# Performance work log

Measured on AMD Instinct MI355X. Metric: run time of the kernel, lower is better.

## Reference

```python
import jax, jax.numpy as jnp
import numpy as np

B, T, V, E = 1024, 100, 9173, 100
H1, H2 = 128, 512


def _gru(x, k, rk, b):
    # Keras GRU v2 (reset_after=True). x: [B,T,D], k: [D,3H], rk: [H,3H], b: [2,3H]
    bi, br = b[0], b[1]
    xs = jnp.swapaxes(jnp.einsum('btd,dh->bth', x, k) + bi, 0, 1)  # [T,B,3H]
    H = rk.shape[0]
    h0 = jnp.zeros((x.shape[0], H), x.dtype)

    def step(h, xt):
        inner = h @ rk + br
        xz, xr, xh = jnp.split(xt, 3, -1)
        rz, rr, rh = jnp.split(inner, 3, -1)
        z = jax.nn.sigmoid(xz + rz)
        r = jax.nn.sigmoid(xr + rr)
        hh = jnp.tanh(xh + r * rh)
        h = z * h + (1.0 - z) * hh
        return h, h

    _, ys = jax.lax.scan(step, h0, xs)
    return jnp.swapaxes(ys, 0, 1)  # [B,T,H]


def _lstm(x, k, rk, b, reverse=False):
    # Keras LSTM, gate order i,f,c,o. x: [B,T,D], k: [D,4H], rk: [H,4H], b: [4H]
    if reverse:
        x = x[:, ::-1]
    xs = jnp.swapaxes(jnp.einsum('btd,dh->bth', x, k) + b, 0, 1)  # [T,B,4H]
    H = rk.shape[0]
    Bb = x.shape[0]
    carry0 = (jnp.zeros((Bb, H), x.dtype), jnp.zeros((Bb, H), x.dtype))

    def step(carry, xt):
        h, c = carry
        g = xt + h @ rk
        i, f, cc, o = jnp.split(g, 4, -1)
        c = jax.nn.sigmoid(f) * c + jax.nn.sigmoid(i) * jnp.tanh(cc)
        h = jax.nn.sigmoid(o) * jnp.tanh(c)
        return (h, c), h

    _, ys = jax.lax.scan(step, carry0, xs)
    ys = jnp.swapaxes(ys, 0, 1)
    if reverse:
        ys = ys[:, ::-1]  # Bidirectional re-reverses backward outputs
    return ys


def setup_inputs() -> dict:
    key = jax.random.key(0)
    ks = jax.random.split(key, 32)
    s = 0.05
    p = {}
    p['text'] = jax.random.randint(ks[0], (B, T), 0, V)
    p['upvote'] = jax.random.normal(ks[1], (B, 1), jnp.float32)
    p['emb'] = s * jax.random.normal(ks[2], (V, E), jnp.float32)
    # forward GRU(128)
    p['gf_k'] = s * jax.random.normal(ks[3], (E, 3 * H1), jnp.float32)
    p['gf_rk'] = s * jax.random.normal(ks[4], (H1, 3 * H1), jnp.float32)
    p['gf_b'] = s * jax.random.normal(ks[5], (2, 3 * H1), jnp.float32)
    # backward LSTM(128)
    p['lb_k'] = s * jax.random.normal(ks[6], (E, 4 * H1), jnp.float32)
    p['lb_rk'] = s * jax.random.normal(ks[7], (H1, 4 * H1), jnp.float32)
    p['lb_b'] = s * jax.random.normal(ks[8], (4 * H1,), jnp.float32)
    # GRU(512) on concat(256)
    p['g2_k'] = s * jax.random.normal(ks[9], (2 * H1, 3 * H2), jnp.float32)
    p['g2_rk'] = s * jax.random.normal(ks[10], (H2, 3 * H2), jnp.float32)
    p['g2_b'] = s * jax.random.normal(ks[11], (2, 3 * H2), jnp.float32)
    # LSTM(512)
    p['l2_k'] = s * jax.random.normal(ks[12], (H2, 4 * H2), jnp.float32)
    p['l2_rk'] = s * jax.random.normal(ks[13], (H2, 4 * H2), jnp.float32)
    p['l2_b'] = s * jax.random.normal(ks[14], (4 * H2,), jnp.float32)
    # dense heads
    p['fc1_w'] = s * jax.random.normal(ks[15], (1, 512), jnp.float32)
    p['fc1_b'] = jnp.zeros((512,), jnp.float32)
    p['d1_w'] = s * jax.random.normal(ks[16], (1024, 64), jnp.float32)
    p['d1_b'] = jnp.zeros((64,), jnp.float32)
    p['d2_w'] = s * jax.random.normal(ks[17], (64, 512), jnp.float32)
    p['d2_b'] = jnp.zeros((512,), jnp.float32)
    p['d3_w'] = s * jax.random.normal(ks[18], (512, 128), jnp.float32)
    p['d3_b'] = jnp.zeros((128,), jnp.float32)
    p['rat_w'] = s * jax.random.normal(ks[19], (128, 5), jnp.float32)
    p['rat_b'] = jnp.zeros((5,), jnp.float32)
    p['rec_w'] = s * jax.random.normal(ks[20], (128, 1), jnp.float32)
    p['rec_b'] = jnp.zeros((1,), jnp.float32)
    return p


def reference(text, upvote, emb, gf_k, gf_rk, gf_b, lb_k, lb_rk, lb_b,
              g2_k, g2_rk, g2_b, l2_k, l2_rk, l2_b,
              fc1_w, fc1_b, d1_w, d1_b, d2_w, d2_b, d3_w, d3_b,
              rat_w, rat_b, rec_w, rec_b):
    x = emb[text]                                   # [B,T,E]
    fwd = _gru(x, gf_k, gf_rk, gf_b)                # [B,T,128]
    bwd = _lstm(x, lb_k, lb_rk, lb_b, reverse=True)  # [B,T,128]
    x1 = jnp.concatenate([fwd, bwd], -1)            # [B,T,256]
    x1 = _gru(x1, g2_k, g2_rk, g2_b)                # [B,T,512]
    x1 = _lstm(x1, l2_k, l2_rk, l2_b)               # [B,T,512]
    x1 = jnp.mean(x1, axis=1)                       # GlobalAveragePooling1D
    x2 = jax.nn.relu(upvote @ fc1_w + fc1_b)        # [B,512]
    h = jnp.concatenate([x1, x2], -1)               # [B,1024]
    h = jax.nn.relu(h @ d1_w + d1_b)
    h = jax.nn.relu(h @ d2_w + d2_b)
    h = jax.nn.relu(h @ d3_w + d3_b)
    rating = jax.nn.softmax(h @ rat_w + rat_b, axis=-1)
    recommend = jax.nn.sigmoid(h @ rec_w + rec_b)
    return rating, recommend
```

## Files before the change

### kernel.cpp

```cpp
#include <hip/hip_runtime.h>

typedef __attribute__((ext_vector_type(8))) short bf16x8;
typedef __attribute__((ext_vector_type(4))) float f32x4;

#define MFMA(a, b, c) __builtin_amdgcn_mfma_f32_16x16x32_bf16((a), (b), (c), 0, 0, 0)

__device__ inline short f2bf(float f) {
  unsigned u = __builtin_bit_cast(unsigned, f);
  u += 0x7fffu + ((u >> 16) & 1u);
  return (short)(u >> 16);
}
__device__ inline float bf2f(short s) {
  unsigned u = ((unsigned)(unsigned short)s) << 16;
  return __builtin_bit_cast(float, u);
}
__device__ inline float sigm(float x) { return 1.f / (1.f + expf(-x)); }

#define B_SZ 1024
#define T_SZ 100

#define O_GFK   0u
#define O_GFRK  (O_GFK  + 98304u)
#define O_LBK   (O_GFRK + 98304u)
#define O_LBRK  (O_LBK  + 131072u)
#define O_G2    (O_LBRK + 131072u)
#define O_L2    (O_G2   + 2359296u)
#define O_X     (O_L2   + 4194304u)
#define O_X1    (O_X    + 26214400u)
#define O_HG    (O_X1   + 52428800u)
#define O_HL    (O_HG   + 2097152u)
#define O_C     (O_HL   + 2097152u)
#define O_MS    (O_C    + 2097152u)

__global__ void pack_b(const float* __restrict__ s1, int K1,
                       const float* __restrict__ s2, int K1p,
                       int Kp, int N, short* __restrict__ dst) {
  int i = blockIdx.x * 256 + threadIdx.x;
  int total = N * Kp;
  if (i >= total) return;
  int v = i & 7, c = (i >> 3) & 15, r = i >> 7;
  int kb8 = Kp >> 3;
  int kb = r % kb8, nt = r / kb8;
  int k = kb * 8 + v, col = nt * 16 + c;
  float val;
  if (k < K1p) val = (k < K1) ? s1[k * N + col] : 0.f;
  else         val = s2[(k - K1p) * N + col];
  dst[i] = f2bf(val);
}

__global__ void embed_k(const int* __restrict__ text, const float* __restrict__ emb,
                        short* __restrict__ x) {
  int i = blockIdx.x * 256 + threadIdx.x;
  if (i >= B_SZ * T_SZ * 128) return;
  int col = i & 127, bt = i >> 7;
  float v = 0.f;
  if (col < 100) v = emb[text[bt] * 100 + col];
  x[i] = f2bf(v);
}

__global__ __launch_bounds__(512) void layer1_k(
    const short* __restrict__ x, const short* __restrict__ gfk,
    const short* __restrict__ gfrk, const float* __restrict__ gfb,
    const short* __restrict__ lbk, const short* __restrict__ lbrk,
    const float* __restrict__ lbb, short* __restrict__ x1) {
  __shared__ __attribute__((aligned(16))) short xst[16 * 136];
  __shared__ __attribute__((aligned(16))) short hst[16 * 136];
  const int wgid = blockIdx.x;
  const bool gru = wgid < 64;
  const int b0 = (gru ? wgid : wgid - 64) * 16;
  const int tid = threadIdx.x, lane = tid & 63, w = tid >> 6;
  const int c = lane & 15, g = lane >> 4;
  const int NS = gru ? 3 : 4;

  for (int i = tid; i < 16 * 136; i += 512) hst[i] = 0;

  const bf16x8* kp = (const bf16x8*)(gru ? gfk : lbk);
  const bf16x8* rp = (const bf16x8*)(gru ? gfrk : lbrk);

  bf16x8 kf[4][4];
  #pragma unroll
  for (int s = 0; s < 4; ++s)
    if (s < NS)
      #pragma unroll
      for (int ks = 0; ks < 4; ++ks)
        kf[s][ks] = kp[((s * 8 + w) * 16 + 4 * ks + g) * 16 + c];

  const int col = w * 16 + c;
  float bz = 0, br_ = 0, bxh = 0, brh = 0, bi_ = 0, bf_ = 0, bc_ = 0, bo_ = 0;
  if (gru) {
    bz  = gfb[col]       + gfb[384 + col];
    br_ = gfb[128 + col] + gfb[512 + col];
    bxh = gfb[256 + col];
    brh = gfb[640 + col];
  } else {
    bi_ = lbb[col]; bf_ = lbb[128 + col]; bc_ = lbb[256 + col]; bo_ = lbb[384 + col];
  }

  float hreg[4] = {0.f, 0.f, 0.f, 0.f};
  float cst[4]  = {0.f, 0.f, 0.f, 0.f};

  for (int tt = 0; tt < T_SZ; ++tt) {
    const int t = gru ? tt : (T_SZ - 1 - tt);
    __syncthreads();
    if (tid < 256) {
      int row = tid >> 4, ch = tid & 15;
      *(bf16x8*)&xst[row * 136 + ch * 8] =
          *(const bf16x8*)&x[((b0 + row) * T_SZ + t) * 128 + ch * 8];
    }
    __syncthreads();

    f32x4 acc[4];
    #pragma unroll
    for (int s = 0; s < 4; ++s) acc[s] = (f32x4){0.f, 0.f, 0.f, 0.f};

    bf16x8 ax[4], ah[4];
    #pragma unroll
    for (int ks = 0; ks < 4; ++ks) {
      ax[ks] = *(const bf16x8*)&xst[c * 136 + ks * 32 + g * 8];
      ah[ks] = *(const bf16x8*)&hst[c * 136 + ks * 32 + g * 8];
    }
    #pragma unroll
    for (int s = 0; s < 4; ++s) {
      if (s < NS) {
        int dst = (gru && s == 2) ? 3 : s;
        #pragma unroll
        for (int ks = 0; ks < 4; ++ks) {
          acc[s] = MFMA(ax[ks], kf[s][ks], acc[s]);
          bf16x8 bh = rp[((s * 8 + w) * 16 + 4 * ks + g) * 16 + c];
          acc[dst] = MFMA(ah[ks], bh, acc[dst]);
        }
      }
    }
    __syncthreads();

    if (gru) {
      #pragma unroll
      for (int j = 0; j < 4; ++j) {
        float z  = sigm(acc[0][j] + bz);
        float r  = sigm(acc[1][j] + br_);
        float hh = tanhf(acc[2][j] + bxh + r * (acc[3][j] + brh));
        float hn = z * hreg[j] + (1.f - z) * hh;
        hreg[j] = hn;
        short hb = f2bf(hn);
        int row = 4 * g + j;
        hst[row * 136 + col] = hb;
        x1[((b0 + row) * T_SZ + t) * 256 + col] = hb;
      }
    } else {
      #pragma unroll
      for (int j = 0; j < 4; ++j) {
        float i_ = acc[0][j] + bi_;
        float f_ = acc[1][j] + bf_;
        float cc = acc[2][j] + bc_;
        float o_ = acc[3][j] + bo_;
        float cn = sigm(f_) * cst[j] + sigm(i_) * tanhf(cc);
        cst[j] = cn;
        float hn = sigm(o_) * tanhf(cn);
        short hb = f2bf(hn);
        int row = 4 * g + j;
        hst[row * 136 + col] = hb;
        x1[((b0 + row) * T_SZ + t) * 256 + 128 + col] = hb;
      }
    }
  }
}

__global__ __launch_bounds__(512) void step_k(
    const short* __restrict__ x1, const short* __restrict__ G2p, const float* __restrict__ g2b,
    const short* __restrict__ L2p, const float* __restrict__ l2b,
    short* __restrict__ hg, short* __restrict__ hl,
    float* __restrict__ cbuf, float* __restrict__ msum, int k) {
  __shared__ __attribute__((aligned(16))) short Ast[64 * 1032];
  const int wgid = blockIdx.x;
  const bool gru = wgid < 128;
  if (gru && k > 99) return;
  if (!gru && k < 1) return;
  const int id = gru ? wgid : wgid - 128;
  const int rowwg = id >> 3, colwg = id & 7;
  const int b0 = rowwg * 64, H0 = colwg * 64;
  const int tid = threadIdx.x, lane = tid & 63, w = tid >> 6;
  const int c = lane & 15, g = lane >> 4;
  const int wm = w >> 2, wn = w & 3;

  if (gru) {
    const int t = k;
    const short* hprev = hg + ((size_t)((k - 1) & 1)) * 524288;
    for (int it = 0; it < 4; ++it) {
      int idx = it * 512 + tid; int row = idx >> 5, ch = idx & 31;
      *(bf16x8*)&Ast[row * 776 + ch * 8] =
          *(const bf16x8*)&x1[((b0 + row) * T_SZ + t) * 256 + ch * 8];
    }
    for (int it = 0; it < 8; ++it) {
      int idx = it * 512 + tid; int row = idx >> 6, ch = idx & 63;
      *(bf16x8*)&Ast[row * 776 + 256 + ch * 8] =
          *(const bf16x8*)&hprev[(b0 + row) * 512 + ch * 8];
    }
    __syncthreads();

    f32x4 acc[2][4];
    #pragma unroll
    for (int mi = 0; mi < 2; ++mi)
      #pragma unroll
      for (int s = 0; s < 4; ++s) acc[mi][s] = (f32x4){0.f, 0.f, 0.f, 0.f};

    const bf16x8* Bp = (const bf16x8*)G2p;
    #pragma unroll 4
    for (int ks = 0; ks < 24; ++ks) {
      bf16x8 a0 = *(const bf16x8*)&Ast[(2 * wm * 16 + c) * 776 + ks * 32 + g * 8];
      bf16x8 a1 = *(const bf16x8*)&Ast[((2 * wm + 1) * 16 + c) * 776 + ks * 32 + g * 8];
      #pragma unroll
      for (int s = 0; s < 3; ++s) {
        int nt = s * 32 + colwg * 4 + wn;
        bf16x8 b = Bp[(nt * 96 + 4 * ks + g) * 16 + c];
        int dst = (s == 2 && ks >= 8) ? 3 : s;
        acc[0][dst] = MFMA(a0, b, acc[0][dst]);
        acc[1][dst] = MFMA(a1, b, acc[1][dst]);
      }
    }

    short* hout = hg + ((size_t)(k & 1)) * 524288;
    const int hcol = H0 + wn * 16 + c;
    #pragma unroll
    for (int mi = 0; mi < 2; ++mi)
      #pragma unroll
      for (int j = 0; j < 4; ++j) {
        int rl = (2 * wm + mi) * 16 + 4 * g + j;
        int rowg = b0 + rl;
        float z  = sigm(acc[mi][0][j] + g2b[hcol] + g2b[1536 + hcol]);
        float r  = sigm(acc[mi][1][j] + g2b[512 + hcol] + g2b[2048 + hcol]);
        float hh = tanhf(acc[mi][2][j] + g2b[1024 + hcol] +
                         r * (acc[mi][3][j] + g2b[2560 + hcol]));
        float hold = bf2f(Ast[rl * 776 + 256 + hcol]);
        float hn = z * hold + (1.f - z) * hh;
        hout[rowg * 512 + hcol] = f2bf(hn);
      }
  } else {
    const int t = k - 1;
    const short* xsrc = hg + ((size_t)(t & 1)) * 524288;
    const short* hprev = hl + ((size_t)((t - 1) & 1)) * 524288;
    for (int it = 0; it < 8; ++it) {
      int idx = it * 512 + tid; int row = idx >> 6, ch = idx & 63;
      *(bf16x8*)&Ast[row * 1032 + ch * 8] =
          *(const bf16x8*)&xsrc[(b0 + row) * 512 + ch * 8];
    }
    for (int it = 0; it < 8; ++it) {
      int idx = it * 512 + tid; int row = idx >> 6, ch = idx & 63;
      *(bf16x8*)&Ast[row * 1032 + 512 + ch * 8] =
          *(const bf16x8*)&hprev[(b0 + row) * 512 + ch * 8];
    }
    __syncthreads();

    f32x4 acc[2][4];
    #pragma unroll
    for (int mi = 0; mi < 2; ++mi)
      #pragma unroll
      for (int s = 0; s < 4; ++s) acc[mi][s] = (f32x4){0.f, 0.f, 0.f, 0.f};

    const bf16x8* Bp = (const bf16x8*)L2p;
    #pragma unroll 4
    for (int ks = 0; ks < 32; ++ks) {
      bf16x8 a0 = *(const bf16x8*)&Ast[(2 * wm * 16 + c) * 1032 + ks * 32 + g * 8];
      bf16x8 a1 = *(const bf16x8*)&Ast[((2 * wm + 1) * 16 + c) * 1032 + ks * 32 + g * 8];
      #pragma unroll
      for (int s = 0; s < 4; ++s) {
        int nt = s * 32 + colwg * 4 + wn;
        bf16x8 b = Bp[(nt * 128 + 4 * ks + g) * 16 + c];
        acc[0][s] = MFMA(a0, b, acc[0][s]);
        acc[1][s] = MFMA(a1, b, acc[1][s]);
      }
    }

    short* hout = hl + ((size_t)(t & 1)) * 524288;
    const int hcol = H0 + wn * 16 + c;
    #pragma unroll
    for (int mi = 0; mi < 2; ++mi)
      #pragma unroll
      for (int j = 0; j < 4; ++j) {
        int rl = (2 * wm + mi) * 16 + 4 * g + j;
        int rowg = b0 + rl;
        int idxg = rowg * 512 + hcol;
        float i_ = acc[mi][0][j] + l2b[hcol];
        float f_ = acc[mi][1][j] + l2b[512 + hcol];
        float cc = acc[mi][2][j] + l2b[1024 + hcol];
        float o_ = acc[mi][3][j] + l2b[1536 + hcol];
        float cn = sigm(f_) * cbuf[idxg] + sigm(i_) * tanhf(cc);
        cbuf[idxg] = cn;
        float hn = sigm(o_) * tanhf(cn);
        hout[idxg] = f2bf(hn);
        msum[idxg] += hn;
      }
  }
}

__global__ __launch_bounds__(256) void head_k(
    const float* __restrict__ msum, const float* __restrict__ upv,
    const float* __restrict__ fc1w, const float* __restrict__ fc1b,
    const float* __restrict__ d1w, const float* __restrict__ d1b,
    const float* __restrict__ d2w, const float* __restrict__ d2b,
    const float* __restrict__ d3w, const float* __restrict__ d3b,
    const float* __restrict__ rw, const float* __restrict__ rb,
    const float* __restrict__ cw, const float* __restrict__ cb,
    float* __restrict__ out) {
  __shared__ float h[1024], o1[64], o2[512], o3[128], lg[8];
  const int b = blockIdx.x, tid = threadIdx.x;
  const float u = upv[b];
  for (int i = tid; i < 512; i += 256) {
    h[i] = msum[b * 512 + i] * 0.01f;
    float v = u * fc1w[i] + fc1b[i];
    h[512 + i] = v > 0.f ? v : 0.f;
  }
  __syncthreads();
  if (tid < 64) {
    float a = d1b[tid];
    for (int i = 0; i < 1024; ++i) a += h[i] * d1w[i * 64 + tid];
    o1[tid] = a > 0.f ? a : 0.f;
  }
  __syncthreads();
  for (int j = tid; j < 512; j += 256) {
    float a = d2b[j];
    for (int i = 0; i < 64; ++i) a += o1[i] * d2w[i * 512 + j];
    o2[j] = a > 0.f ? a : 0.f;
  }
  __syncthreads();
  if (tid < 128) {
    float a = d3b[tid];
    for (int i = 0; i < 512; ++i) a += o2[i] * d3w[i * 128 + tid];
    o3[tid] = a > 0.f ? a : 0.f;
  }
  __syncthreads();
  if (tid < 5) {
    float a = rb[tid];
    for (int i = 0; i < 128; ++i) a += o3[i] * rw[i * 5 + tid];
    lg[tid] = a;
  }
  if (tid == 5) {
    float a = cb[0];
    for (int i = 0; i < 128; ++i) a += o3[i] * cw[i];
    out[5120 + b] = 1.f / (1.f + expf(-a));
  }
  __syncthreads();
  if (tid == 0) {
    float m = lg[0];
    for (int j = 1; j < 5; ++j) m = fmaxf(m, lg[j]);
    float e[5], s = 0.f;
    for (int j = 0; j < 5; ++j) { e[j] = expf(lg[j] - m); s += e[j]; }
    for (int j = 0; j < 5; ++j) out[b * 5 + j] = e[j] / s;
  }
}

extern "C" void kernel_launch(void* const* d_in, const int* in_sizes, int n_in,
                              void* d_out, int out_size, void* d_ws, size_t ws_size,
                              hipStream_t stream) {
  const int*   text  = (const int*)  d_in[0];
  const float* upv   = (const float*)d_in[1];
  const float* emb   = (const float*)d_in[2];
  const float* gf_k  = (const float*)d_in[3];
  const float* gf_rk = (const float*)d_in[4];
  const float* gf_b  = (const float*)d_in[5];
  const float* lb_k  = (const float*)d_in[6];
  const float* lb_rk = (const float*)d_in[7];
  const float* lb_b  = (const float*)d_in[8];
  const float* g2_k  = (const float*)d_in[9];
  const float* g2_rk = (const float*)d_in[10];
  const float* g2_b  = (const float*)d_in[11];
  const float* l2_k  = (const float*)d_in[12];
  const float* l2_rk = (const float*)d_in[13];
  const float* l2_b  = (const float*)d_in[14];
  const float* fc1_w = (const float*)d_in[15];
  const float* fc1_b = (const float*)d_in[16];
  const float* d1_w  = (const float*)d_in[17];
  const float* d1_b  = (const float*)d_in[18];
  const float* d2_w  = (const float*)d_in[19];
  const float* d2_b  = (const float*)d_in[20];
  const float* d3_w  = (const float*)d_in[21];
  const float* d3_b  = (const float*)d_in[22];
  const float* rat_w = (const float*)d_in[23];
  const float* rat_b = (const float*)d_in[24];
  const float* rec_w = (const float*)d_in[25];
  const float* rec_b = (const float*)d_in[26];

  char* ws = (char*)d_ws;
  short* gfkp  = (short*)(ws + O_GFK);
  short* gfrkp = (short*)(ws + O_GFRK);
  short* lbkp  = (short*)(ws + O_LBK);
  short* lbrkp = (short*)(ws + O_LBRK);
  short* G2p   = (short*)(ws + O_G2);
  short* L2p   = (short*)(ws + O_L2);
  short* xb    = (short*)(ws + O_X);
  short* x1    = (short*)(ws + O_X1);
  short* hg    = (short*)(ws + O_HG);
  short* hl    = (short*)(ws + O_HL);
  float* cbuf  = (float*)(ws + O_C);
  float* msum  = (float*)(ws + O_MS);

  pack_b<<<192, 256, 0, stream>>>(gf_k, 100, gf_k, 128, 128, 384, gfkp);
  pack_b<<<192, 256, 0, stream>>>(gf_rk, 128, gf_rk, 128, 128, 384, gfrkp);
  pack_b<<<256, 256, 0, stream>>>(lb_k, 100, lb_k, 128, 128, 512, lbkp);
  pack_b<<<256, 256, 0, stream>>>(lb_rk, 128, lb_rk, 128, 128, 512, lbrkp);
  pack_b<<<4608, 256, 0, stream>>>(g2_k, 256, g2_rk, 256, 768, 1536, G2p);
  pack_b<<<8192, 256, 0, stream>>>(l2_k, 512, l2_rk, 512, 1024, 2048, L2p);

  embed_k<<<51200, 256, 0, stream>>>(text, emb, xb);

  hipMemsetAsync(ws + O_HG + 1048576u, 0, 1048576u, stream);
  hipMemsetAsync(ws + O_HL + 1048576u, 0, 1048576u, stream);
  hipMemsetAsync(ws + O_C, 0, 2097152u, stream);
  hipMemsetAsync(ws + O_MS, 0, 2097152u, stream);

  layer1_k<<<128, 512, 0, stream>>>(xb, gfkp, gfrkp, gf_b, lbkp, lbrkp, lb_b, x1);

  for (int k = 0; k <= 100; ++k)
    step_k<<<256, 512, 0, stream>>>(x1, G2p, g2_b, L2p, l2_b, hg, hl, cbuf, msum, k);

  head_k<<<1024, 256, 0, stream>>>(msum, upv, fc1_w, fc1_b, d1_w, d1_b, d2_w, d2_b,
                                   d3_w, d3_b, rat_w, rat_b, rec_w, rec_b,
                                   (float*)d_out);
}
```

Measured before the change: 3.226 ms.

## Replace per-timestep launches with a persistent cooperative kernel using a grid barrier

```diff
diff --git a/kernel.cpp b/kernel.cpp
--- a/kernel.cpp
+++ b/kernel.cpp
@@ -29,8 +29,8 @@
 #define O_X1    (O_X    + 26214400u)
 #define O_HG    (O_X1   + 52428800u)
 #define O_HL    (O_HG   + 2097152u)
-#define O_C     (O_HL   + 2097152u)
-#define O_MS    (O_C    + 2097152u)
+#define O_BAR   (O_HL   + 2097152u)
+#define O_MS    (O_BAR  + 2097152u)
 
 __global__ void pack_b(const float* __restrict__ s1, int K1,
                        const float* __restrict__ s2, int K1p,
@@ -63,6 +63,7 @@
     const short* __restrict__ gfrk, const float* __restrict__ gfb,
     const short* __restrict__ lbk, const short* __restrict__ lbrk,
     const float* __restrict__ lbb, short* __restrict__ x1) {
+  __shared__ __attribute__((aligned(16))) short rkl[65536];
   __shared__ __attribute__((aligned(16))) short xst[16 * 136];
   __shared__ __attribute__((aligned(16))) short hst[16 * 136];
   const int wgid = blockIdx.x;
@@ -75,7 +76,13 @@
   for (int i = tid; i < 16 * 136; i += 512) hst[i] = 0;
 
   const bf16x8* kp = (const bf16x8*)(gru ? gfk : lbk);
-  const bf16x8* rp = (const bf16x8*)(gru ? gfrk : lbrk);
+  const bf16x8* rpg = (const bf16x8*)(gru ? gfrk : lbrk);
+  {
+    bf16x8* rl8 = (bf16x8*)rkl;
+    int n8 = gru ? 6144 : 8192;
+    for (int i = tid; i < n8; i += 512) rl8[i] = rpg[i];
+  }
+  const bf16x8* rp = (const bf16x8*)rkl;
 
   bf16x8 kf[4][4];
   #pragma unroll
@@ -165,131 +172,205 @@
   }
 }
 
-__global__ __launch_bounds__(512) void step_k(
+__device__ __forceinline__ void gbar(unsigned* cnt, unsigned* rel, int gen) {
+  __syncthreads();
+  if (threadIdx.x == 0) {
+    __threadfence();
+    unsigned old = __hip_atomic_fetch_add(cnt, 1u, __ATOMIC_ACQ_REL, __HIP_MEMORY_SCOPE_AGENT);
+    unsigned want = (unsigned)(gen + 1);
+    if (old == want * 256u - 1u) {
+      __hip_atomic_store(rel, want, __ATOMIC_RELEASE, __HIP_MEMORY_SCOPE_AGENT);
+    } else {
+      unsigned tries = 0;
+      while (__hip_atomic_load(rel, __ATOMIC_ACQUIRE, __HIP_MEMORY_SCOPE_AGENT) < want) {
+        __builtin_amdgcn_s_sleep(2);
+        if (++tries > (1u << 22)) break;
+      }
+    }
+    __threadfence();
+  }
+  __syncthreads();
+}
+
+__global__ __launch_bounds__(512, 2) void persist2_k(
     const short* __restrict__ x1, const short* __restrict__ G2p, const float* __restrict__ g2b,
     const short* __restrict__ L2p, const float* __restrict__ l2b,
     short* __restrict__ hg, short* __restrict__ hl,
-    float* __restrict__ cbuf, float* __restrict__ msum, int k) {
-  __shared__ __attribute__((aligned(16))) short Ast[64 * 1032];
+    float* __restrict__ msum, unsigned* __restrict__ bar) {
+  __shared__ __attribute__((aligned(16))) short Asm[65536];
+  float* XA = (float*)&Asm[0];
+  float* XB = (float*)&Asm[49152];
+
   const int wgid = blockIdx.x;
-  const bool gru = wgid < 128;
-  if (gru && k > 99) return;
-  if (!gru && k < 1) return;
-  const int id = gru ? wgid : wgid - 128;
-  const int rowwg = id >> 3, colwg = id & 7;
-  const int b0 = rowwg * 64, H0 = colwg * 64;
-  const int tid = threadIdx.x, lane = tid & 63, w = tid >> 6;
+  const int rowwg = wgid >> 4, colwg = wgid & 15;
+  const int b0 = rowwg * 64;
+  const int tid = threadIdx.x, w = tid >> 6, lane = tid & 63;
   const int c = lane & 15, g = lane >> 4;
-  const int wm = w >> 2, wn = w & 3;
-
-  if (gru) {
-    const int t = k;
-    const short* hprev = hg + ((size_t)((k - 1) & 1)) * 524288;
-    for (int it = 0; it < 4; ++it) {
-      int idx = it * 512 + tid; int row = idx >> 5, ch = idx & 31;
-      *(bf16x8*)&Ast[row * 776 + ch * 8] =
-          *(const bf16x8*)&x1[((b0 + row) * T_SZ + t) * 256 + ch * 8];
-    }
-    for (int it = 0; it < 8; ++it) {
-      int idx = it * 512 + tid; int row = idx >> 6, ch = idx & 63;
-      *(bf16x8*)&Ast[row * 776 + 256 + ch * 8] =
-          *(const bf16x8*)&hprev[(b0 + row) * 512 + ch * 8];
-    }
-    __syncthreads();
-
-    f32x4 acc[2][4];
+  const int sw = (c & 7) << 3;
+  const int ehc = lane & 31;
+  const int er0 = w * 8 + (lane >> 5) * 4;
+  const int hcg = colwg * 32 + ehc;
+
+  const float bz  = g2b[hcg] + g2b[1536 + hcg];
+  const float br_ = g2b[512 + hcg] + g2b[2048 + hcg];
+  const float bxh = g2b[1024 + hcg];
+  const float brh = g2b[2560 + hcg];
+  const float bi_ = l2b[hcg], bf_ = l2b[512 + hcg];
+  const float bc_ = l2b[1024 + hcg], bo_ = l2b[1536 + hcg];
+
+  const int lgate = w & 3, lkh = w >> 2;
+  const bf16x8* L2v = (const bf16x8*)L2p;
+  bf16x8 lb[16][2];
+  #pragma unroll
+  for (int ks = 0; ks < 16; ++ks)
     #pragma unroll
-    for (int mi = 0; mi < 2; ++mi)
-      #pragma unroll
-      for (int s = 0; s < 4; ++s) acc[mi][s] = (f32x4){0.f, 0.f, 0.f, 0.f};
-
-    const bf16x8* Bp = (const bf16x8*)G2p;
-    #pragma unroll 4
-    for (int ks = 0; ks < 24; ++ks) {
-      bf16x8 a0 = *(const bf16x8*)&Ast[(2 * wm * 16 + c) * 776 + ks * 32 + g * 8];
-      bf16x8 a1 = *(const bf16x8*)&Ast[((2 * wm + 1) * 16 + c) * 776 + ks * 32 + g * 8];
-      #pragma unroll
-      for (int s = 0; s < 3; ++s) {
-        int nt = s * 32 + colwg * 4 + wn;
-        bf16x8 b = Bp[(nt * 96 + 4 * ks + g) * 16 + c];
-        int dst = (s == 2 && ks >= 8) ? 3 : s;
-        acc[0][dst] = MFMA(a0, b, acc[0][dst]);
-        acc[1][dst] = MFMA(a1, b, acc[1][dst]);
-      }
-    }
-
-    short* hout = hg + ((size_t)(k & 1)) * 524288;
-    const int hcol = H0 + wn * 16 + c;
-    #pragma unroll
-    for (int mi = 0; mi < 2; ++mi)
+    for (int n = 0; n < 2; ++n)
+      lb[ks][n] = L2v[((size_t)(lgate * 32 + colwg * 2 + n) * 128 + 4 * (lkh * 16 + ks) + g) * 16 + c];
+
+  const bf16x8* Gv = (const bf16x8*)G2p;
+  const int gw = w >> 1, ghf = w & 1;
+  const int gntg = gw * 32 + colwg * 2 + ghf;
+
+  float creg[4] = {0.f, 0.f, 0.f, 0.f};
+  float mreg[4] = {0.f, 0.f, 0.f, 0.f};
+
+  for (int k = 0; k <= 100; ++k) {
+    const short* hg_rd = hg + (size_t)((k + 1) & 1) * 524288;
+
+    if (k < 100) {
+      const bf16x8* x1v = (const bf16x8*)x1;
+      const bf16x8* hgp8 = (const bf16x8*)hg_rd;
+      for (int it = 0; it < 12; ++it) {
+        int idx = it * 512 + tid;
+        int row = idx / 96;
+        int c16 = idx - row * 96;
+        bf16x8 v = (c16 < 32)
+            ? x1v[((size_t)(b0 + row) * T_SZ + k) * 32 + c16]
+            : hgp8[(size_t)(b0 + row) * 64 + (c16 - 32)];
+        *(bf16x8*)&Asm[row * 768 + (c16 ^ (row & 7)) * 8] = v;
+      }
+      __syncthreads();
+
+      if (w < 6) {
+        f32x4 acc[4], acch[4];
+        #pragma unroll
+        for (int m = 0; m < 4; ++m) {
+          acc[m] = (f32x4){0.f, 0.f, 0.f, 0.f};
+          acch[m] = (f32x4){0.f, 0.f, 0.f, 0.f};
+        }
+        #pragma unroll 6
+        for (int ks = 0; ks < 24; ++ks) {
+          bf16x8 b = Gv[((size_t)gntg * 96 + 4 * ks + g) * 16 + c];
+          bf16x8 a[4];
+          #pragma unroll
+          for (int m = 0; m < 4; ++m)
+            a[m] = *(const bf16x8*)&Asm[(m * 16 + c) * 768 + ((ks * 32 + g * 8) ^ sw)];
+          if (w >= 4 && ks >= 8) {
+            #pragma unroll
+            for (int m = 0; m < 4; ++m) acch[m] = MFMA(a[m], b, acch[m]);
+          } else {
+            #pragma unroll
+            for (int m = 0; m < 4; ++m) acc[m] = MFMA(a[m], b, acc[m]);
+          }
+        }
+        #pragma unroll
+        for (int m = 0; m < 4; ++m)
+          #pragma unroll
+          for (int j = 0; j < 4; ++j) {
+            int row = m * 16 + 4 * g + j;
+            if (gw < 2) XB[(gw * 64 + row) * 32 + ghf * 16 + c] = acc[m][j];
+            else {
+              XB[(2 * 64 + row) * 32 + ghf * 16 + c] = acc[m][j];
+              XB[(3 * 64 + row) * 32 + ghf * 16 + c] = acch[m][j];
+            }
+          }
+      }
+      __syncthreads();
+
+      short* hgw = hg + (size_t)(k & 1) * 524288;
       #pragma unroll
       for (int j = 0; j < 4; ++j) {
-        int rl = (2 * wm + mi) * 16 + 4 * g + j;
-        int rowg = b0 + rl;
-        float z  = sigm(acc[mi][0][j] + g2b[hcol] + g2b[1536 + hcol]);
-        float r  = sigm(acc[mi][1][j] + g2b[512 + hcol] + g2b[2048 + hcol]);
-        float hh = tanhf(acc[mi][2][j] + g2b[1024 + hcol] +
-                         r * (acc[mi][3][j] + g2b[2560 + hcol]));
-        float hold = bf2f(Ast[rl * 776 + 256 + hcol]);
+        int r = er0 + j;
+        int xi = r * 32 + ehc;
+        float z  = sigm(XB[xi] + bz);
+        float rr = sigm(XB[xi + 2048] + br_);
+        float hh = tanhf(XB[xi + 4096] + bxh + rr * (XB[xi + 6144] + brh));
+        int hi = 256 + hcg;
+        int hswz = ((((hi >> 3) ^ (r & 7)) << 3) | (hi & 7));
+        float hold = bf2f(Asm[r * 768 + hswz]);
         float hn = z * hold + (1.f - z) * hh;
-        hout[rowg * 512 + hcol] = f2bf(hn);
-      }
-  } else {
-    const int t = k - 1;
-    const short* xsrc = hg + ((size_t)(t & 1)) * 524288;
-    const short* hprev = hl + ((size_t)((t - 1) & 1)) * 524288;
-    for (int it = 0; it < 8; ++it) {
-      int idx = it * 512 + tid; int row = idx >> 6, ch = idx & 63;
-      *(bf16x8*)&Ast[row * 1032 + ch * 8] =
-          *(const bf16x8*)&xsrc[(b0 + row) * 512 + ch * 8];
-    }
-    for (int it = 0; it < 8; ++it) {
-      int idx = it * 512 + tid; int row = idx >> 6, ch = idx & 63;
-      *(bf16x8*)&Ast[row * 1032 + 512 + ch * 8] =
-          *(const bf16x8*)&hprev[(b0 + row) * 512 + ch * 8];
-    }
-    __syncthreads();
-
-    f32x4 acc[2][4];
-    #pragma unroll
-    for (int mi = 0; mi < 2; ++mi)
-      #pragma unroll
-      for (int s = 0; s < 4; ++s) acc[mi][s] = (f32x4){0.f, 0.f, 0.f, 0.f};
-
-    const bf16x8* Bp = (const bf16x8*)L2p;
-    #pragma unroll 4
-    for (int ks = 0; ks < 32; ++ks) {
-      bf16x8 a0 = *(const bf16x8*)&Ast[(2 * wm * 16 + c) * 1032 + ks * 32 + g * 8];
-      bf16x8 a1 = *(const bf16x8*)&Ast[((2 * wm + 1) * 16 + c) * 1032 + ks * 32 + g * 8];
-      #pragma unroll
-      for (int s = 0; s < 4; ++s) {
-        int nt = s * 32 + colwg * 4 + wn;
-        bf16x8 b = Bp[(nt * 128 + 4 * ks + g) * 16 + c];
-        acc[0][s] = MFMA(a0, b, acc[0][s]);
-        acc[1][s] = MFMA(a1, b, acc[1][s]);
-      }
-    }
-
-    short* hout = hl + ((size_t)(t & 1)) * 524288;
-    const int hcol = H0 + wn * 16 + c;
-    #pragma unroll
-    for (int mi = 0; mi < 2; ++mi)
+        hgw[(size_t)(b0 + r) * 512 + hcg] = f2bf(hn);
+      }
+      __syncthreads();
+    }
+
+    if (k >= 1) {
+      const bf16x8* xs8 = (const bf16x8*)hg_rd;
+      const bf16x8* hp8 = (const bf16x8*)(hl + (size_t)(k & 1) * 524288);
+      for (int it = 0; it < 16; ++it) {
+        int idx = it * 512 + tid;
+        int row = idx >> 7;
+        int c16 = idx & 127;
+        bf16x8 v = (c16 < 64)
+            ? xs8[(size_t)(b0 + row) * 64 + c16]
+            : hp8[(size_t)(b0 + row) * 64 + (c16 - 64)];
+        *(bf16x8*)&Asm[row * 1024 + (c16 ^ (row & 7)) * 8] = v;
+      }
+      __syncthreads();
+
+      f32x4 acc[4][2];
+      #pragma unroll
+      for (int m = 0; m < 4; ++m)
+        #pragma unroll
+        for (int n = 0; n < 2; ++n) acc[m][n] = (f32x4){0.f, 0.f, 0.f, 0.f};
+
+      #pragma unroll
+      for (int ks = 0; ks < 16; ++ks) {
+        bf16x8 a[4];
+        #pragma unroll
+        for (int m = 0; m < 4; ++m)
+          a[m] = *(const bf16x8*)&Asm[(m * 16 + c) * 1024 + ((lkh * 512 + ks * 32 + g * 8) ^ sw)];
+        #pragma unroll
+        for (int m = 0; m < 4; ++m)
+          #pragma unroll
+          for (int n = 0; n < 2; ++n)
+            acc[m][n] = MFMA(a[m], lb[ks][n], acc[m][n]);
+      }
+      __syncthreads();
+
+      float* Xp = lkh ? XB : XA;
+      #pragma unroll
+      for (int m = 0; m < 4; ++m)
+        #pragma unroll
+        for (int n = 0; n < 2; ++n)
+          #pragma unroll
+          for (int j = 0; j < 4; ++j)
+            Xp[(lgate * 64 + m * 16 + 4 * g + j) * 32 + n * 16 + c] = acc[m][n][j];
+      __syncthreads();
+
+      short* hlw = hl + (size_t)((k + 1) & 1) * 524288;
       #pragma unroll
       for (int j = 0; j < 4; ++j) {
-        int rl = (2 * wm + mi) * 16 + 4 * g + j;
-        int rowg = b0 + rl;
-        int idxg = rowg * 512 + hcol;
-        float i_ = acc[mi][0][j] + l2b[hcol];
-        float f_ = acc[mi][1][j] + l2b[512 + hcol];
-        float cc = acc[mi][2][j] + l2b[1024 + hcol];
-        float o_ = acc[mi][3][j] + l2b[1536 + hcol];
-        float cn = sigm(f_) * cbuf[idxg] + sigm(i_) * tanhf(cc);
-        cbuf[idxg] = cn;
+        int r = er0 + j;
+        int xi = r * 32 + ehc;
+        float i_ = XA[xi]        + XB[xi]        + bi_;
+        float f_ = XA[xi + 2048] + XB[xi + 2048] + bf_;
+        float cc = XA[xi + 4096] + XB[xi + 4096] + bc_;
+        float o_ = XA[xi + 6144] + XB[xi + 6144] + bo_;
+        float cn = sigm(f_) * creg[j] + sigm(i_) * tanhf(cc);
+        creg[j] = cn;
         float hn = sigm(o_) * tanhf(cn);
-        hout[idxg] = f2bf(hn);
-        msum[idxg] += hn;
-      }
-  }
+        mreg[j] += hn;
+        hlw[(size_t)(b0 + r) * 512 + hcg] = f2bf(hn);
+      }
+    }
+
+    gbar(bar, bar + 16, k);
+  }
+
+  #pragma unroll
+  for (int j = 0; j < 4; ++j)
+    msum[(size_t)(b0 + er0 + j) * 512 + hcg] = mreg[j];
 }
 
 __global__ __launch_bounds__(256) void head_k(
@@ -390,7 +471,7 @@
   short* x1    = (short*)(ws + O_X1);
   short* hg    = (short*)(ws + O_HG);
   short* hl    = (short*)(ws + O_HL);
-  float* cbuf  = (float*)(ws + O_C);
+  unsigned* bar = (unsigned*)(ws + O_BAR);
   float* msum  = (float*)(ws + O_MS);
 
   pack_b<<<192, 256, 0, stream>>>(gf_k, 100, gf_k, 128, 128, 384, gfkp);
@@ -404,13 +485,21 @@
 
   hipMemsetAsync(ws + O_HG + 1048576u, 0, 1048576u, stream);
   hipMemsetAsync(ws + O_HL + 1048576u, 0, 1048576u, stream);
-  hipMemsetAsync(ws + O_C, 0, 2097152u, stream);
-  hipMemsetAsync(ws + O_MS, 0, 2097152u, stream);
+  hipMemsetAsync(ws + O_BAR, 0, 256u, stream);
 
   layer1_k<<<128, 512, 0, stream>>>(xb, gfkp, gfrkp, gf_b, lbkp, lbrkp, lb_b, x1);
 
-  for (int k = 0; k <= 100; ++k)
-    step_k<<<256, 512, 0, stream>>>(x1, G2p, g2_b, L2p, l2_b, hg, hl, cbuf, msum, k);
+  {
+    const short* x1c = x1; const short* G2c = G2p; const short* L2c = L2p;
+    void* kargs[] = {(void*)&x1c, (void*)&G2c, (void*)&g2_b, (void*)&L2c, (void*)&l2_b,
+                     (void*)&hg, (void*)&hl, (void*)&msum, (void*)&bar};
+    hipError_t e = hipLaunchCooperativeKernel((void*)persist2_k, dim3(256), dim3(512),
+                                              kargs, 0, stream);
+    if (e != hipSuccess) {
+      (void)hipGetLastError();
+      persist2_k<<<256, 512, 0, stream>>>(x1c, G2c, g2_b, L2c, l2_b, hg, hl, msum, bar);
+    }
+  }
 
   head_k<<<1024, 256, 0, stream>>>(msum, upv, fc1_w, fc1_b, d1_w, d1_b, d2_w, d2_b,
                                    d3_w, d3_b, rat_w, rat_b, rec_w, rec_b,
```

Result: slower. 6.766 ms (+109.7%).
